# Kernel tuning notes

Hardware: AMD Instinct MI355X
Metric: run time of the kernel (lower is better)

The kernel has to match this reference:

```python
import jax, jax.numpy as jnp
import numpy as np

OUTCOMES = [8, 8, 8, 8, 8, 8]           # concept outcome counts (concepts_order)
N_TOTAL = int(np.prod(OUTCOMES))        # 262144 joint states
N_VALID = 8192                          # admissible states
B, D = 4096, 1024


def setup_inputs() -> dict:
    key = jax.random.key(0)
    k1, k2 = jax.random.split(key)
    embeddings = jax.random.normal(k1, (B, D), dtype=jnp.float32)
    W = jax.random.normal(k2, (N_VALID, D), dtype=jnp.float32) * 0.02
    b = jnp.zeros((N_VALID,), dtype=jnp.float32)
    # unique sorted admissible-state indices, like torch.argwhere(mask)
    rng = np.random.default_rng(0)
    valid_states = jnp.asarray(
        np.sort(rng.choice(N_TOTAL, size=N_VALID, replace=False)).astype(np.int32))
    return {"embeddings": embeddings, "W": W, "b": b, "valid_states": valid_states}


def reference(embeddings, W, b, valid_states):
    # softmax over valid states: [B, N_VALID]
    probs = jax.nn.softmax(embeddings @ W.T + b, axis=1)
    probs_t = probs.T  # [N_VALID, B] for leading-axis segment reduction
    marginals = []
    stride = N_TOTAL
    for n_i in OUTCOMES:
        stride //= n_i
        # digit of each valid joint-state index along this concept's axis
        digit = (valid_states // stride) % n_i  # [N_VALID]
        # equivalent to scattering probs into the full joint tensor and
        # summing over all other concept axes, without materializing it
        m = jax.ops.segment_sum(probs_t, digit, num_segments=n_i).T  # [B, n_i]
        marginals.append(m)
    return jnp.stack(marginals)  # [n_concepts, B, 8]
```

## Files before the change

### kernel.cpp

```cpp
#include <hip/hip_runtime.h>
#include <hip/hip_bf16.h>
#include <cstdint>
#include <cstddef>

typedef __bf16 bf16_t;
typedef bf16_t bf16x8 __attribute__((ext_vector_type(8)));
typedef bf16_t bf16x4 __attribute__((ext_vector_type(4)));
typedef float  f32x4  __attribute__((ext_vector_type(4)));
typedef unsigned int u32;

#define BROWS 4096
#define NV    8192
#define KD    1024
#define NT    16
#define ST    48
#define LOG2E 1.44269504088896340736f

#define GLL(gsrc, ldst) \
  __builtin_amdgcn_global_load_lds((const __attribute__((address_space(1))) u32*)(gsrc), \
                                   (__attribute__((address_space(3))) u32*)(ldst), 16, 0, 0)
#define FENCE asm volatile("" ::: "memory")

__global__ void cvt_kernel(const float* __restrict__ src, bf16_t* __restrict__ dst, int n4) {
  int idx = blockIdx.x * blockDim.x + threadIdx.x;
  int stride = gridDim.x * blockDim.x;
  for (int i = idx; i < n4; i += stride) {
    float4 v = ((const float4*)src)[i];
    bf16x4 o;
    o[0] = (bf16_t)v.x; o[1] = (bf16_t)v.y; o[2] = (bf16_t)v.z; o[3] = (bf16_t)v.w;
    ((bf16x4*)dst)[i] = o;
  }
}

__global__ void build_s2t_kernel(const int* __restrict__ vstate, bf16_t* __restrict__ s2t) {
  int g = blockIdx.x * blockDim.x + threadIdx.x;
  if (g >= ST * NV) return;
  int b = g >> 13;
  int ig = g & (NV - 1);
  int c = b >> 3;
  int d = b & 7;
  int src = ig ^ ((b & 7) << 3);
  int dig = (vstate[src] >> (15 - 3 * c)) & 7;
  s2t[g] = (bf16_t)(dig == d ? 1.0f : 0.0f);
}

__global__ __launch_bounds__(512, 2)
void gemm_fused_kernel(const bf16_t* __restrict__ W, const bf16_t* __restrict__ E,
                       const float* __restrict__ bias, const bf16_t* __restrict__ s2t,
                       float* __restrict__ part) {
  __shared__ __align__(16) char lds[2][65536];
  #define AKH0 0
  #define AKH1 16384
  #define BKH0 32768
  #define BKH1 49152

  const int t    = threadIdx.x;
  const int lane = t & 63;
  const int wv   = t >> 6;
  const int wm   = wv >> 2;
  const int wn   = wv & 3;
  const int fr   = lane & 15;
  const int fq   = lane >> 4;

  int bid = blockIdx.x;
  int wg  = (bid & 7) * 64 + (bid >> 3);
  const int stile = wg >> 4;
  const int btile = wg & 15;
  const int st0 = stile * 256;
  const int bt0 = btile * 256;

  const int srow = lane >> 2;
  const int skel = ((lane & 3) ^ ((lane >> 3) & 3)) * 8;
  const bf16_t* aptr = W + (size_t)(st0 + wv * 32 + srow) * KD + skel;
  const bf16_t* bptr = E + (size_t)(bt0 + wv * 32 + srow) * KD + skel;
  const int dchunk = (wv * 2) * 1024;

  const int xsw = (fr & 6) << 3;
  const int base_a = (((wm * 128 + fr) * 64 + fq * 16) ^ xsw);
  const int base_b = 32768 + (((wn * 64 + fr) * 64 + fq * 16) ^ xsw);

  f32x4 acc[8][4] = {};

  GLL(aptr, &lds[0][AKH0 + dchunk]);
  GLL(aptr + 16 * KD, &lds[0][AKH0 + dchunk + 1024]);
  GLL(bptr, &lds[0][BKH0 + dchunk]);
  GLL(bptr + 16 * KD, &lds[0][BKH0 + dchunk + 1024]);
  GLL(aptr + 32, &lds[0][AKH1 + dchunk]);
  GLL(aptr + 32 + 16 * KD, &lds[0][AKH1 + dchunk + 1024]);
  GLL(bptr + 32, &lds[0][BKH1 + dchunk]);
  GLL(bptr + 32 + 16 * KD, &lds[0][BKH1 + dchunk + 1024]);
  asm volatile("s_waitcnt vmcnt(0)" ::: "memory");
  __builtin_amdgcn_s_barrier();
  FENCE;

  int cur = 0;
  for (int kt = 0; kt < NT; ++kt) {
    const char* bufp = lds[cur];
    char* nbuf = lds[cur ^ 1];
    const bool pf = (kt + 1 < NT);

    bf16x8 a0[8], b0[4], a1[8], b1[4];

#pragma unroll
    for (int n = 0; n < 4; ++n)
      b0[n] = *(const bf16x8*)(bufp + base_b + n * 1024);
#pragma unroll
    for (int m = 0; m < 8; ++m)
      a0[m] = *(const bf16x8*)(bufp + base_a + m * 1024);

    if (pf) {
      const bf16_t* an = aptr + (kt + 1) * 64;
      const bf16_t* bn = bptr + (kt + 1) * 64;
      GLL(an, &nbuf[AKH0 + dchunk]);
      GLL(an + 16 * KD, &nbuf[AKH0 + dchunk + 1024]);
      GLL(bn, &nbuf[BKH0 + dchunk]);
      GLL(bn + 16 * KD, &nbuf[BKH0 + dchunk + 1024]);
      GLL(an + 32, &nbuf[AKH1 + dchunk]);
      GLL(an + 32 + 16 * KD, &nbuf[AKH1 + dchunk + 1024]);
      GLL(bn + 32, &nbuf[BKH1 + dchunk]);
      GLL(bn + 32 + 16 * KD, &nbuf[BKH1 + dchunk + 1024]);
    }

#pragma unroll
    for (int n = 0; n < 4; ++n)
      b1[n] = *(const bf16x8*)(bufp + base_b + 16384 + n * 1024);
#pragma unroll
    for (int m = 0; m < 8; ++m)
      a1[m] = *(const bf16x8*)(bufp + base_a + 16384 + m * 1024);

    __builtin_amdgcn_s_setprio(1);
#pragma unroll
    for (int m = 0; m < 8; ++m)
#pragma unroll
      for (int n = 0; n < 4; ++n)
        acc[m][n] = __builtin_amdgcn_mfma_f32_16x16x32_bf16(a0[m], b0[n], acc[m][n], 0, 0, 0);
#pragma unroll
    for (int m = 0; m < 8; ++m)
#pragma unroll
      for (int n = 0; n < 4; ++n)
        acc[m][n] = __builtin_amdgcn_mfma_f32_16x16x32_bf16(a1[m], b1[n], acc[m][n], 0, 0, 0);
    __builtin_amdgcn_s_setprio(0);

    asm volatile("s_waitcnt vmcnt(0)" ::: "memory");
    __builtin_amdgcn_sched_barrier(0);
    __builtin_amdgcn_s_barrier();
    FENCE;
    cur ^= 1;
  }

  char* const ldsf = &lds[0][0];
  {
#pragma unroll
    for (int q = 0; q < 3; ++q) {
      const bf16_t* src = s2t + (size_t)(wv * 6 + q * 2 + (lane >> 5)) * NV
                          + st0 + (lane & 31) * 8;
      GLL(src, ldsf + 65536 + wv * 3072 + q * 1024);
    }
  }

  float* const ppart = part + ((size_t)stile * BROWS + bt0) * ST;

#pragma unroll
  for (int pass = 0; pass < 2; ++pass) {
    if ((wn >> 1) == pass) {
#pragma unroll
      for (int m = 0; m < 8; ++m) {
        const float4 bb = *(const float4*)&bias[st0 + wm * 128 + m * 16 + fq * 4];
#pragma unroll
        for (int n = 0; n < 4; ++n) {
          bf16x4 ev;
          ev[0] = (bf16_t)exp2f((acc[m][n][0] + bb.x) * LOG2E);
          ev[1] = (bf16_t)exp2f((acc[m][n][1] + bb.y) * LOG2E);
          ev[2] = (bf16_t)exp2f((acc[m][n][2] + bb.z) * LOG2E);
          ev[3] = (bf16_t)exp2f((acc[m][n][3] + bb.w) * LOG2E);
          const int jh = (wn & 1) * 64 + n * 16 + fr;
          const int ib = (wm * 128 + m * 16 + fq * 4) * 2;
          *(bf16x4*)(ldsf + jh * 512 + (ib ^ ((fr & 7) << 4))) = ev;
        }
      }
    }
    if (pass == 0) asm volatile("s_waitcnt vmcnt(0)" ::: "memory");
    __syncthreads();

    f32x4 acc2[3] = {{0.f,0.f,0.f,0.f},{0.f,0.f,0.f,0.f},{0.f,0.f,0.f,0.f}};
#pragma unroll
    for (int k2 = 0; k2 < 8; ++k2) {
      const int ko = (k2 * 64 + fq * 16) ^ ((fr & 7) << 4);
      const bf16x8 ea = *(const bf16x8*)(ldsf + (wv * 16 + fr) * 512 + ko);
#pragma unroll
      for (int n2 = 0; n2 < 3; ++n2) {
        const bf16x8 sb = *(const bf16x8*)(ldsf + 65536 + (n2 * 16 + fr) * 512 + ko);
        acc2[n2] = __builtin_amdgcn_mfma_f32_16x16x32_bf16(ea, sb, acc2[n2], 0, 0, 0);
      }
    }
    const int jg = pass * 128 + wv * 16 + fq * 4;
#pragma unroll
    for (int n2 = 0; n2 < 3; ++n2)
#pragma unroll
      for (int r = 0; r < 4; ++r)
        ppart[(size_t)(jg + r) * ST + n2 * 16 + fr] = acc2[n2][r];
    __syncthreads();
  }
}

__global__ __launch_bounds__(64)
void reduce_kernel(const float* __restrict__ part, float* __restrict__ out) {
  const int b = blockIdx.x;
  const int t = threadIdx.x;
  __shared__ float fin[ST];
  if (t < ST) {
    float s = 0.f;
#pragma unroll
    for (int mt = 0; mt < 32; ++mt)
      s += part[((size_t)mt * BROWS + b) * ST + t];
    fin[t] = s;
  }
  __syncthreads();
  if (t < ST) {
    float total = fin[0] + fin[1] + fin[2] + fin[3] + fin[4] + fin[5] + fin[6] + fin[7];
    out[(size_t)(t >> 3) * BROWS * 8 + (size_t)b * 8 + (t & 7)] = fin[t] / total;
  }
}

extern "C" void kernel_launch(void* const* d_in, const int* in_sizes, int n_in,
                              void* d_out, int out_size, void* d_ws, size_t ws_size,
                              hipStream_t stream) {
  const float* E    = (const float*)d_in[0];
  const float* W    = (const float*)d_in[1];
  const float* bias = (const float*)d_in[2];
  const int*   vs   = (const int*)d_in[3];
  float* out = (float*)d_out;

  char* ws = (char*)d_ws;
  size_t off = 0;
  bf16_t* Eb   = (bf16_t*)(ws + off); off += (size_t)BROWS * KD * 2;
  bf16_t* Wb   = (bf16_t*)(ws + off); off += (size_t)NV * KD * 2;
  bf16_t* s2t  = (bf16_t*)(ws + off); off += (size_t)ST * NV * 2;
  float*  part = (float*)(ws + off);  off += (size_t)32 * BROWS * ST * 4;

  build_s2t_kernel<<<(ST * NV + 255) / 256, 256, 0, stream>>>(vs, s2t);
  cvt_kernel<<<2048, 256, 0, stream>>>(E, Eb, BROWS * KD / 4);
  cvt_kernel<<<2048, 256, 0, stream>>>(W, Wb, NV * KD / 4);
  gemm_fused_kernel<<<512, 512, 0, stream>>>(Wb, Eb, bias, s2t, part);
  reduce_kernel<<<BROWS, 64, 0, stream>>>(part, out);
}
```

Before: 106.2 us.

## Use 32x32x16 MFMA, fuse prep kernels, unswizzle s2t, transpose partials layout

Switches the main GEMM from 16x16x32 to 32x32x16 bf16 MFMA tiles with a matching LDS read layout, which cuts the number of LDS fragment loads per MFMA. The three prep kernels (two casts plus s2t build) are merged into one launch, and s2t is now built unswizzled with vectorized writes. The s2t tile is staged through registers into padded LDS rows instead of an async global-to-LDS copy. The partial-sum layout is changed so the reduce kernel reads contiguous memory. Several independent changes land at once, and the padded 592-byte LDS stride together with the new exp write pattern could introduce bank conflicts.

```diff
diff --git a/kernel.cpp b/kernel.cpp
--- a/kernel.cpp
+++ b/kernel.cpp
@@ -7,6 +7,7 @@
 typedef bf16_t bf16x8 __attribute__((ext_vector_type(8)));
 typedef bf16_t bf16x4 __attribute__((ext_vector_type(4)));
 typedef float  f32x4  __attribute__((ext_vector_type(4)));
+typedef float  f32x16 __attribute__((ext_vector_type(16)));
 typedef unsigned int u32;
 
 #define BROWS 4096
@@ -21,27 +22,37 @@
                                    (__attribute__((address_space(3))) u32*)(ldst), 16, 0, 0)
 #define FENCE asm volatile("" ::: "memory")
 
-__global__ void cvt_kernel(const float* __restrict__ src, bf16_t* __restrict__ dst, int n4) {
+__global__ void prep_kernel(const float* __restrict__ E, const float* __restrict__ W,
+                            const int* __restrict__ vs,
+                            bf16_t* __restrict__ Eb, bf16_t* __restrict__ Wb,
+                            bf16_t* __restrict__ s2t) {
+  const int nE = BROWS * KD / 4;
+  const int nW = NV * KD / 4;
+  const int nS = ST * NV / 8;
+  const int nT = nE + nW + nS;
   int idx = blockIdx.x * blockDim.x + threadIdx.x;
   int stride = gridDim.x * blockDim.x;
-  for (int i = idx; i < n4; i += stride) {
-    float4 v = ((const float4*)src)[i];
-    bf16x4 o;
-    o[0] = (bf16_t)v.x; o[1] = (bf16_t)v.y; o[2] = (bf16_t)v.z; o[3] = (bf16_t)v.w;
-    ((bf16x4*)dst)[i] = o;
-  }
-}
-
-__global__ void build_s2t_kernel(const int* __restrict__ vstate, bf16_t* __restrict__ s2t) {
-  int g = blockIdx.x * blockDim.x + threadIdx.x;
-  if (g >= ST * NV) return;
-  int b = g >> 13;
-  int ig = g & (NV - 1);
-  int c = b >> 3;
-  int d = b & 7;
-  int src = ig ^ ((b & 7) << 3);
-  int dig = (vstate[src] >> (15 - 3 * c)) & 7;
-  s2t[g] = (bf16_t)(dig == d ? 1.0f : 0.0f);
+  for (int i = idx; i < nT; i += stride) {
+    if (i < nE + nW) {
+      const float4* s; bf16x4* d; int j;
+      if (i < nE) { s = (const float4*)E; d = (bf16x4*)Eb; j = i; }
+      else        { s = (const float4*)W; d = (bf16x4*)Wb; j = i - nE; }
+      float4 v = s[j];
+      bf16x4 o;
+      o[0] = (bf16_t)v.x; o[1] = (bf16_t)v.y; o[2] = (bf16_t)v.z; o[3] = (bf16_t)v.w;
+      d[j] = o;
+    } else {
+      int u  = i - nE - nW;
+      int b  = u >> 10;
+      int i0 = (u & 1023) * 8;
+      int c = b >> 3, d = b & 7, sh = 15 - 3 * c;
+      bf16x8 o;
+#pragma unroll
+      for (int e = 0; e < 8; ++e)
+        o[e] = (bf16_t)((((vs[i0 + e] >> sh) & 7) == d) ? 1.0f : 0.0f);
+      *(bf16x8*)(s2t + (size_t)b * NV + i0) = o;
+    }
+  }
 }
 
 __global__ __launch_bounds__(512, 2)
@@ -53,6 +64,7 @@
   #define AKH1 16384
   #define BKH0 32768
   #define BKH1 49152
+  #define SOFF 75776
 
   const int t    = threadIdx.x;
   const int lane = t & 63;
@@ -61,6 +73,8 @@
   const int wn   = wv & 3;
   const int fr   = lane & 15;
   const int fq   = lane >> 4;
+  const int l31  = lane & 31;
+  const int hi   = lane >> 5;
 
   int bid = blockIdx.x;
   int wg  = (bid & 7) * 64 + (bid >> 3);
@@ -75,19 +89,19 @@
   const bf16_t* bptr = E + (size_t)(bt0 + wv * 32 + srow) * KD + skel;
   const int dchunk = (wv * 2) * 1024;
 
-  const int xsw = (fr & 6) << 3;
-  const int base_a = (((wm * 128 + fr) * 64 + fq * 16) ^ xsw);
-  const int base_b = 32768 + (((wn * 64 + fr) * 64 + fq * 16) ^ xsw);
-
-  f32x4 acc[8][4] = {};
-
-  GLL(aptr, &lds[0][AKH0 + dchunk]);
-  GLL(aptr + 16 * KD, &lds[0][AKH0 + dchunk + 1024]);
-  GLL(bptr, &lds[0][BKH0 + dchunk]);
-  GLL(bptr + 16 * KD, &lds[0][BKH0 + dchunk + 1024]);
-  GLL(aptr + 32, &lds[0][AKH1 + dchunk]);
+  const int inner  = (hi * 16) ^ ((l31 & 6) << 3);
+  const int a_base = wm * 8192 + l31 * 64 + inner;
+  const int b_base = wn * 4096 + l31 * 64 + inner;
+
+  f32x16 acc[4][2] = {};
+
+  GLL(aptr,                &lds[0][AKH0 + dchunk]);
+  GLL(aptr + 16 * KD,      &lds[0][AKH0 + dchunk + 1024]);
+  GLL(bptr,                &lds[0][BKH0 + dchunk]);
+  GLL(bptr + 16 * KD,      &lds[0][BKH0 + dchunk + 1024]);
+  GLL(aptr + 32,           &lds[0][AKH1 + dchunk]);
   GLL(aptr + 32 + 16 * KD, &lds[0][AKH1 + dchunk + 1024]);
-  GLL(bptr + 32, &lds[0][BKH1 + dchunk]);
+  GLL(bptr + 32,           &lds[0][BKH1 + dchunk]);
   GLL(bptr + 32 + 16 * KD, &lds[0][BKH1 + dchunk + 1024]);
   asm volatile("s_waitcnt vmcnt(0)" ::: "memory");
   __builtin_amdgcn_s_barrier();
@@ -99,46 +113,58 @@
     char* nbuf = lds[cur ^ 1];
     const bool pf = (kt + 1 < NT);
 
-    bf16x8 a0[8], b0[4], a1[8], b1[4];
-
-#pragma unroll
-    for (int n = 0; n < 4; ++n)
-      b0[n] = *(const bf16x8*)(bufp + base_b + n * 1024);
-#pragma unroll
-    for (int m = 0; m < 8; ++m)
-      a0[m] = *(const bf16x8*)(bufp + base_a + m * 1024);
+    bf16x8 a0[4][2], b0[2][2], a1[4][2], b1[2][2];
+
+#pragma unroll
+    for (int n = 0; n < 2; ++n)
+#pragma unroll
+      for (int ks = 0; ks < 2; ++ks)
+        b0[n][ks] = *(const bf16x8*)(bufp + BKH0 + (b_base ^ (ks << 5)) + n * 2048);
+#pragma unroll
+    for (int m = 0; m < 4; ++m)
+#pragma unroll
+      for (int ks = 0; ks < 2; ++ks)
+        a0[m][ks] = *(const bf16x8*)(bufp + AKH0 + (a_base ^ (ks << 5)) + m * 2048);
 
     if (pf) {
       const bf16_t* an = aptr + (kt + 1) * 64;
       const bf16_t* bn = bptr + (kt + 1) * 64;
-      GLL(an, &nbuf[AKH0 + dchunk]);
-      GLL(an + 16 * KD, &nbuf[AKH0 + dchunk + 1024]);
-      GLL(bn, &nbuf[BKH0 + dchunk]);
-      GLL(bn + 16 * KD, &nbuf[BKH0 + dchunk + 1024]);
-      GLL(an + 32, &nbuf[AKH1 + dchunk]);
+      GLL(an,                &nbuf[AKH0 + dchunk]);
+      GLL(an + 16 * KD,      &nbuf[AKH0 + dchunk + 1024]);
+      GLL(bn,                &nbuf[BKH0 + dchunk]);
+      GLL(bn + 16 * KD,      &nbuf[BKH0 + dchunk + 1024]);
+      GLL(an + 32,           &nbuf[AKH1 + dchunk]);
       GLL(an + 32 + 16 * KD, &nbuf[AKH1 + dchunk + 1024]);
-      GLL(bn + 32, &nbuf[BKH1 + dchunk]);
+      GLL(bn + 32,           &nbuf[BKH1 + dchunk]);
       GLL(bn + 32 + 16 * KD, &nbuf[BKH1 + dchunk + 1024]);
     }
 
 #pragma unroll
-    for (int n = 0; n < 4; ++n)
-      b1[n] = *(const bf16x8*)(bufp + base_b + 16384 + n * 1024);
-#pragma unroll
-    for (int m = 0; m < 8; ++m)
-      a1[m] = *(const bf16x8*)(bufp + base_a + 16384 + m * 1024);
+    for (int n = 0; n < 2; ++n)
+#pragma unroll
+      for (int ks = 0; ks < 2; ++ks)
+        b1[n][ks] = *(const bf16x8*)(bufp + BKH1 + (b_base ^ (ks << 5)) + n * 2048);
+#pragma unroll
+    for (int m = 0; m < 4; ++m)
+#pragma unroll
+      for (int ks = 0; ks < 2; ++ks)
+        a1[m][ks] = *(const bf16x8*)(bufp + AKH1 + (a_base ^ (ks << 5)) + m * 2048);
 
     __builtin_amdgcn_s_setprio(1);
 #pragma unroll
-    for (int m = 0; m < 8; ++m)
-#pragma unroll
-      for (int n = 0; n < 4; ++n)
-        acc[m][n] = __builtin_amdgcn_mfma_f32_16x16x32_bf16(a0[m], b0[n], acc[m][n], 0, 0, 0);
-#pragma unroll
-    for (int m = 0; m < 8; ++m)
-#pragma unroll
-      for (int n = 0; n < 4; ++n)
-        acc[m][n] = __builtin_amdgcn_mfma_f32_16x16x32_bf16(a1[m], b1[n], acc[m][n], 0, 0, 0);
+    for (int ks = 0; ks < 2; ++ks)
+#pragma unroll
+      for (int m = 0; m < 4; ++m)
+#pragma unroll
+        for (int n = 0; n < 2; ++n)
+          acc[m][n] = __builtin_amdgcn_mfma_f32_32x32x16_bf16(a0[m][ks], b0[n][ks], acc[m][n], 0, 0, 0);
+#pragma unroll
+    for (int ks = 0; ks < 2; ++ks)
+#pragma unroll
+      for (int m = 0; m < 4; ++m)
+#pragma unroll
+        for (int n = 0; n < 2; ++n)
+          acc[m][n] = __builtin_amdgcn_mfma_f32_32x32x16_bf16(a1[m][ks], b1[n][ks], acc[m][n], 0, 0, 0);
     __builtin_amdgcn_s_setprio(0);
 
     asm volatile("s_waitcnt vmcnt(0)" ::: "memory");
@@ -149,47 +175,51 @@
   }
 
   char* const ldsf = &lds[0][0];
-  {
-#pragma unroll
-    for (int q = 0; q < 3; ++q) {
-      const bf16_t* src = s2t + (size_t)(wv * 6 + q * 2 + (lane >> 5)) * NV
-                          + st0 + (lane & 31) * 8;
-      GLL(src, ldsf + 65536 + wv * 3072 + q * 1024);
-    }
-  }
-
-  float* const ppart = part + ((size_t)stile * BROWS + bt0) * ST;
+
+  bf16x8 sreg[3];
+#pragma unroll
+  for (int q = 0; q < 3; ++q) {
+    const int c = t * 3 + q;
+    sreg[q] = *(const bf16x8*)(s2t + (size_t)(c >> 5) * NV + st0 + (c & 31) * 8);
+  }
+
+  float* const ppart = part + (size_t)bt0 * (32 * ST) + (size_t)stile * ST;
 
 #pragma unroll
   for (int pass = 0; pass < 2; ++pass) {
     if ((wn >> 1) == pass) {
-#pragma unroll
-      for (int m = 0; m < 8; ++m) {
-        const float4 bb = *(const float4*)&bias[st0 + wm * 128 + m * 16 + fq * 4];
-#pragma unroll
-        for (int n = 0; n < 4; ++n) {
-          bf16x4 ev;
-          ev[0] = (bf16_t)exp2f((acc[m][n][0] + bb.x) * LOG2E);
-          ev[1] = (bf16_t)exp2f((acc[m][n][1] + bb.y) * LOG2E);
-          ev[2] = (bf16_t)exp2f((acc[m][n][2] + bb.z) * LOG2E);
-          ev[3] = (bf16_t)exp2f((acc[m][n][3] + bb.w) * LOG2E);
-          const int jh = (wn & 1) * 64 + n * 16 + fr;
-          const int ib = (wm * 128 + m * 16 + fq * 4) * 2;
-          *(bf16x4*)(ldsf + jh * 512 + (ib ^ ((fr & 7) << 4))) = ev;
-        }
+      const int j = (wn & 1) * 64 + l31;
+#pragma unroll
+      for (int m = 0; m < 4; ++m)
+#pragma unroll
+        for (int n = 0; n < 2; ++n)
+#pragma unroll
+          for (int g = 0; g < 4; ++g) {
+            const float4 bb = *(const float4*)&bias[st0 + wm * 128 + m * 32 + g * 8 + hi * 4];
+            bf16x4 ev;
+            ev[0] = (bf16_t)exp2f((acc[m][n][g * 4 + 0] + bb.x) * LOG2E);
+            ev[1] = (bf16_t)exp2f((acc[m][n][g * 4 + 1] + bb.y) * LOG2E);
+            ev[2] = (bf16_t)exp2f((acc[m][n][g * 4 + 2] + bb.z) * LOG2E);
+            ev[3] = (bf16_t)exp2f((acc[m][n][g * 4 + 3] + bb.w) * LOG2E);
+            *(bf16x4*)(ldsf + (j + n * 32) * 592 + wm * 256 + m * 64 + g * 16 + hi * 8) = ev;
+          }
+    }
+    if (pass == 0) {
+#pragma unroll
+      for (int q = 0; q < 3; ++q) {
+        const int c = t * 3 + q;
+        *(bf16x8*)(ldsf + SOFF + (c >> 5) * 592 + (c & 31) * 16) = sreg[q];
       }
     }
-    if (pass == 0) asm volatile("s_waitcnt vmcnt(0)" ::: "memory");
     __syncthreads();
 
     f32x4 acc2[3] = {{0.f,0.f,0.f,0.f},{0.f,0.f,0.f,0.f},{0.f,0.f,0.f,0.f}};
 #pragma unroll
     for (int k2 = 0; k2 < 8; ++k2) {
-      const int ko = (k2 * 64 + fq * 16) ^ ((fr & 7) << 4);
-      const bf16x8 ea = *(const bf16x8*)(ldsf + (wv * 16 + fr) * 512 + ko);
+      const bf16x8 ea = *(const bf16x8*)(ldsf + (wv * 16 + fr) * 592 + k2 * 64 + fq * 16);
 #pragma unroll
       for (int n2 = 0; n2 < 3; ++n2) {
-        const bf16x8 sb = *(const bf16x8*)(ldsf + 65536 + (n2 * 16 + fr) * 512 + ko);
+        const bf16x8 sb = *(const bf16x8*)(ldsf + SOFF + (n2 * 16 + fr) * 592 + k2 * 64 + fq * 16);
         acc2[n2] = __builtin_amdgcn_mfma_f32_16x16x32_bf16(ea, sb, acc2[n2], 0, 0, 0);
       }
     }
@@ -198,7 +228,7 @@
     for (int n2 = 0; n2 < 3; ++n2)
 #pragma unroll
       for (int r = 0; r < 4; ++r)
-        ppart[(size_t)(jg + r) * ST + n2 * 16 + fr] = acc2[n2][r];
+        ppart[(size_t)(jg + r) * (32 * ST) + n2 * 16 + fr] = acc2[n2][r];
     __syncthreads();
   }
 }
@@ -209,10 +239,11 @@
   const int t = threadIdx.x;
   __shared__ float fin[ST];
   if (t < ST) {
+    const float* p = part + (size_t)b * (32 * ST) + t;
     float s = 0.f;
 #pragma unroll
     for (int mt = 0; mt < 32; ++mt)
-      s += part[((size_t)mt * BROWS + b) * ST + t];
+      s += p[mt * ST];
     fin[t] = s;
   }
   __syncthreads();
@@ -236,11 +267,9 @@
   bf16_t* Eb   = (bf16_t*)(ws + off); off += (size_t)BROWS * KD * 2;
   bf16_t* Wb   = (bf16_t*)(ws + off); off += (size_t)NV * KD * 2;
   bf16_t* s2t  = (bf16_t*)(ws + off); off += (size_t)ST * NV * 2;
-  float*  part = (float*)(ws + off);  off += (size_t)32 * BROWS * ST * 4;
-
-  build_s2t_kernel<<<(ST * NV + 255) / 256, 256, 0, stream>>>(vs, s2t);
-  cvt_kernel<<<2048, 256, 0, stream>>>(E, Eb, BROWS * KD / 4);
-  cvt_kernel<<<2048, 256, 0, stream>>>(W, Wb, NV * KD / 4);
+  float*  part = (float*)(ws + off);  off += (size_t)BROWS * 32 * ST * 4;
+
+  prep_kernel<<<3072, 256, 0, stream>>>(E, W, vs, Eb, Wb, s2t);
   gemm_fused_kernel<<<512, 512, 0, stream>>>(Wb, Eb, bias, s2t, part);
   reduce_kernel<<<BROWS, 64, 0, stream>>>(part, out);
 }
```

Measured after the change: 109.1 us. 1.03x slower.
